# Kernel tuning notes

Measured on AMD Instinct MI355X. Metric: run time of the kernel, lower is better.

The kernel has to match this reference:

```python
import jax, jax.numpy as jnp
import numpy as np

N = 100000
EMB = 64
HID = 64
E = 1600000

def _sage_conv(x, src, dst, w_l, b_l, w_r):
    # PyG SAGEConv (aggr='mean'): out_i = lin_l(mean_{j->i} x_j) + lin_r(x_i)
    msgs = x[src]                                        # [E, d] gather
    agg = jax.ops.segment_sum(msgs, dst, num_segments=N) # [N, d] scatter-add
    deg = jax.ops.segment_sum(jnp.ones((src.shape[0],), x.dtype), dst, num_segments=N)
    agg = agg / jnp.maximum(deg, 1.0)[:, None]           # mean; 0-degree nodes stay 0
    return agg @ w_l.T + b_l + x @ w_r.T                 # lin_l has bias, lin_r does not

def setup_inputs() -> dict:
    key = jax.random.key(0)
    ks = jax.random.split(key, 8)
    emb_std = 1.0 / (EMB ** 0.5)
    # Linear init (Kaiming-uniform-like bounds approximated with uniform +-1/sqrt(fan_in))
    def lin(k, out_d, in_d):
        return jax.random.uniform(k, (out_d, in_d), jnp.float32, -1.0/np.sqrt(in_d), 1.0/np.sqrt(in_d))
    return {
        "embedding": jax.random.normal(ks[0], (N, EMB), jnp.float32) * emb_std,
        "w_l0": lin(ks[1], HID, EMB),
        "b_l0": jax.random.uniform(ks[2], (HID,), jnp.float32, -1.0/np.sqrt(EMB), 1.0/np.sqrt(EMB)),
        "w_r0": lin(ks[3], HID, EMB),
        "w_l1": lin(ks[4], HID, HID),
        "b_l1": jax.random.uniform(ks[5], (HID,), jnp.float32, -1.0/np.sqrt(HID), 1.0/np.sqrt(HID)),
        "w_r1": lin(ks[6], HID, HID),
        "edge_index": jax.random.randint(ks[7], (2, E), 0, N, dtype=jnp.int64),
    }

def reference(embedding, w_l0, b_l0, w_r0, w_l1, b_l1, w_r1, edge_index):
    src, dst = edge_index[0], edge_index[1]
    x = embedding
    x = _sage_conv(x, src, dst, w_l0, b_l0, w_r0)
    x = jax.nn.relu(x)
    x = _sage_conv(x, src, dst, w_l1, b_l1, w_r1)
    # F.normalize(p=2, dim=1): x / clamp_min(||x||_2, 1e-12)
    norm = jnp.sqrt(jnp.sum(x * x, axis=1, keepdims=True))
    return x / jnp.maximum(norm, 1e-12)
```

## Files before the change

kernel.cpp:

```cpp
#include <hip/hip_runtime.h>
#include <math.h>

#define D 64
#define BSHIFT 9
#define BN 512
#define MAXB 256
#define NBLK 256
#define NBLK_LOG 8
#define SCHUNK 4096

typedef short bf16x8v __attribute__((ext_vector_type(8)));
typedef float f32x4v __attribute__((ext_vector_type(4)));

__device__ __forceinline__ unsigned short f2bf(float f) {
    unsigned u = __float_as_uint(f);
    return (unsigned short)((u + 0x7FFFu + ((u >> 16) & 1u)) >> 16);
}
__device__ __forceinline__ float bf2f(unsigned short b) {
    return __uint_as_float(((unsigned)b) << 16);
}

__global__ void detect_idx64(const int* __restrict__ ei, int* __restrict__ flag) {
    int v = ei[2 * threadIdx.x + 1];
    unsigned long long b = __ballot(v != 0);
    if (threadIdx.x == 0) flag[0] = (b == 0ULL) ? 1 : 0;
}

__global__ __launch_bounds__(256) void conv_w4(
        const float* __restrict__ w0, const float* __restrict__ w1,
        const float* __restrict__ w2, const float* __restrict__ w3,
        unsigned short* __restrict__ hi, unsigned short* __restrict__ lo) {
    int i = blockIdx.x * 256 + threadIdx.x;
    const float* ws_[4] = {w0, w1, w2, w3};
    float f = ws_[i >> 12][i & 4095];
    unsigned short h = f2bf(f);
    hi[i] = h;
    lo[i] = f2bf(f - bf2f(h));
}

__global__ __launch_bounds__(256) void conv_xbf(
        const float* __restrict__ x, uint4* __restrict__ xb4, int total8) {
    int i = blockIdx.x * 256 + threadIdx.x;
    int stride = gridDim.x * 256;
    for (; i < total8; i += stride) {
        float4 u0 = *(const float4*)(x + (size_t)i * 8);
        float4 u1 = *(const float4*)(x + (size_t)i * 8 + 4);
        uint4 p;
        p.x = (unsigned)f2bf(u0.x) | ((unsigned)f2bf(u0.y) << 16);
        p.y = (unsigned)f2bf(u0.z) | ((unsigned)f2bf(u0.w) << 16);
        p.z = (unsigned)f2bf(u1.x) | ((unsigned)f2bf(u1.y) << 16);
        p.w = (unsigned)f2bf(u1.z) | ((unsigned)f2bf(u1.w) << 16);
        xb4[i] = p;
    }
}


__global__ __launch_bounds__(256) void hist2d(
        const void* __restrict__ eidx, const int* __restrict__ flagp,
        int* __restrict__ H, int nE, int nb, int epb) {
    __shared__ int h[MAXB];
    const bool idx64 = (*flagp != 0);
    const int* __restrict__ ei32 = (const int*)eidx;
    const long long* __restrict__ ei64 = (const long long*)eidx;
    for (int i = threadIdx.x; i < nb; i += 256) h[i] = 0;
    __syncthreads();
    const int e0 = blockIdx.x * epb;
    const int e1 = min(e0 + epb, nE);
    for (int e = e0 + threadIdx.x; e < e1; e += 256) {
        int d = idx64 ? (int)ei64[e + nE] : ei32[e + nE];
        atomicAdd(&h[d >> BSHIFT], 1);
    }
    __syncthreads();
    for (int i = threadIdx.x; i < nb; i += 256)
        H[(i << NBLK_LOG) + blockIdx.x] = h[i];
}

__global__ __launch_bounds__(256) void scan_h_partial(
        const int* __restrict__ H, int* __restrict__ part, int total) {
    __shared__ int red[4];
    int base = blockIdx.x * SCHUNK + threadIdx.x * 16;
    int s = 0;
    #pragma unroll
    for (int k = 0; k < 16; ++k) { int i = base + k; if (i < total) s += H[i]; }
    #pragma unroll
    for (int off = 32; off >= 1; off >>= 1) s += __shfl_xor(s, off, 64);
    int lane = threadIdx.x & 63, wid = threadIdx.x >> 6;
    if (lane == 0) red[wid] = s;
    __syncthreads();
    if (threadIdx.x == 0) part[blockIdx.x] = red[0] + red[1] + red[2] + red[3];
}

__global__ void scan_h_mid(int* __restrict__ part, int* __restrict__ bbaseN,
                           int nParts, int nE) {
    int tid = threadIdx.x;
    int v = (tid < nParts) ? part[tid] : 0;
    int x = v;
    #pragma unroll
    for (int off = 1; off < 64; off <<= 1) { int y = __shfl_up(x, off, 64); if (tid >= off) x += y; }
    if (tid < nParts) part[tid] = x - v;
    if (tid == 0) bbaseN[0] = nE;
}

__global__ __launch_bounds__(256) void scan_h_final(
        int* __restrict__ H, const int* __restrict__ part,
        int* __restrict__ bbase, int total) {
    __shared__ int wtot[4];
    int tid = threadIdx.x, lane = tid & 63, wid = tid >> 6;
    int base = blockIdx.x * SCHUNK + tid * 16;
    int v[16]; int t = 0;
    #pragma unroll
    for (int k = 0; k < 16; ++k) { int i = base + k; v[k] = (i < total) ? H[i] : 0; t += v[k]; }
    int x = t;
    #pragma unroll
    for (int off = 1; off < 64; off <<= 1) { int y = __shfl_up(x, off, 64); if (lane >= off) x += y; }
    if (lane == 63) wtot[wid] = x;
    __syncthreads();
    int woff = 0;
    for (int w = 0; w < wid; ++w) woff += wtot[w];
    int run = part[blockIdx.x] + woff + (x - t);
    #pragma unroll
    for (int k = 0; k < 16; ++k) {
        int i = base + k;
        if (i < total) {
            H[i] = run;
            if ((i & (NBLK - 1)) == 0) bbase[i >> NBLK_LOG] = run;
            run += v[k];
        }
    }
}

__global__ __launch_bounds__(256) void fill2(
        const void* __restrict__ eidx, const int* __restrict__ flagp,
        const int* __restrict__ H, unsigned* __restrict__ pairs,
        int nE, int nb, int epb) {
    __shared__ int cur[MAXB];
    const bool idx64 = (*flagp != 0);
    const int* __restrict__ ei32 = (const int*)eidx;
    const long long* __restrict__ ei64 = (const long long*)eidx;
    for (int i = threadIdx.x; i < nb; i += 256)
        cur[i] = H[(i << NBLK_LOG) + blockIdx.x];
    __syncthreads();
    const int e0 = blockIdx.x * epb;
    const int e1 = min(e0 + epb, nE);
    for (int e = e0 + threadIdx.x; e < e1; e += 256) {
        int s, d;
        if (idx64) { s = (int)ei64[e]; d = (int)ei64[e + nE]; }
        else       { s = ei32[e];      d = ei32[e + nE]; }
        int pos = atomicAdd(&cur[d >> BSHIFT], 1);
        pairs[pos] = (unsigned)s | ((unsigned)(d & (BN - 1)) << 20);
    }
}

__global__ __launch_bounds__(512) void bucket_to_csr(
        const unsigned* __restrict__ pairs,
        const int* __restrict__ bbase,
        int* __restrict__ rowStart, int* __restrict__ srcs,
        int N, int nb, int nE) {
    __shared__ int lcnt[BN];
    __shared__ int lcur[BN];
    __shared__ int wtot[8];
    const int b = blockIdx.x;
    const int base = bbase[b];
    const int cnt  = bbase[b + 1] - base;
    const int tid = threadIdx.x, lane = tid & 63, wid = tid >> 6;
    lcnt[tid] = 0;
    __syncthreads();
    for (int i = tid; i < cnt; i += 512)
        atomicAdd(&lcnt[(int)(pairs[base + i] >> 20)], 1);
    __syncthreads();
    int v = lcnt[tid];
    int x = v;
    #pragma unroll
    for (int off = 1; off < 64; off <<= 1) { int y = __shfl_up(x, off, 64); if (lane >= off) x += y; }
    if (lane == 63) wtot[wid] = x;
    __syncthreads();
    if (tid == 0) {
        int r = 0;
        for (int w = 0; w < 8; ++w) { int t = wtot[w]; wtot[w] = r; r += t; }
    }
    __syncthreads();
    int excl = wtot[wid] + (x - v);
    lcur[tid] = excl;
    int node = b * BN + tid;
    if (node < N) rowStart[node] = base + excl;
    if (b == nb - 1 && tid == 0) rowStart[N] = nE;
    __syncthreads();
    for (int i = tid; i < cnt; i += 512) {
        unsigned p = pairs[base + i];
        int pos = atomicAdd(&lcur[(int)(p >> 20)], 1);
        srcs[base + pos] = (int)(p & 0xFFFFFu);
    }
}

#define UNPK8(v, arr)                                                     \
    do {                                                                  \
        arr[0] += __uint_as_float((v).x << 16);                           \
        arr[1] += __uint_as_float((v).x & 0xFFFF0000u);                   \
        arr[2] += __uint_as_float((v).y << 16);                           \
        arr[3] += __uint_as_float((v).y & 0xFFFF0000u);                   \
        arr[4] += __uint_as_float((v).z << 16);                           \
        arr[5] += __uint_as_float((v).z & 0xFFFF0000u);                   \
        arr[6] += __uint_as_float((v).w << 16);                           \
        arr[7] += __uint_as_float((v).w & 0xFFFF0000u);                   \
    } while (0)

__global__ __launch_bounds__(256) void gather_mean_bf16(
        const unsigned short* __restrict__ xb,
        const int* __restrict__ rowStart,
        const int* __restrict__ srcs,
        unsigned short* __restrict__ aggb,
        int nNodes) {
    const int tid = threadIdx.x;
    const int gl = tid & 7;
    const int grp = tid >> 3;
    const int node = blockIdx.x * 32 + grp;
    if (node >= nNodes) return;
    const int r0 = rowStart[node], r1 = rowStart[node + 1];
    float a[8] = {0.f,0.f,0.f,0.f,0.f,0.f,0.f,0.f};
    const unsigned short* xp = xb + gl * 8;
    int j = r0;
    for (; j + 4 <= r1; j += 4) {
        int s0 = srcs[j], s1 = srcs[j + 1], s2 = srcs[j + 2], s3 = srcs[j + 3];
        uint4 v0 = *(const uint4*)(xp + (size_t)s0 * D);
        uint4 v1 = *(const uint4*)(xp + (size_t)s1 * D);
        uint4 v2 = *(const uint4*)(xp + (size_t)s2 * D);
        uint4 v3 = *(const uint4*)(xp + (size_t)s3 * D);
        UNPK8(v0, a); UNPK8(v1, a); UNPK8(v2, a); UNPK8(v3, a);
    }
    if (j + 2 <= r1) {
        int s0 = srcs[j], s1 = srcs[j + 1];
        uint4 v0 = *(const uint4*)(xp + (size_t)s0 * D);
        uint4 v1 = *(const uint4*)(xp + (size_t)s1 * D);
        UNPK8(v0, a); UNPK8(v1, a);
        j += 2;
    }
    if (j < r1) {
        uint4 v = *(const uint4*)(xp + (size_t)srcs[j] * D);
        UNPK8(v, a);
    }
    const float inv = 1.0f / fmaxf((float)(r1 - r0), 1.0f);
    uint4 p;
    p.x = (unsigned)f2bf(a[0]*inv) | ((unsigned)f2bf(a[1]*inv) << 16);
    p.y = (unsigned)f2bf(a[2]*inv) | ((unsigned)f2bf(a[3]*inv) << 16);
    p.z = (unsigned)f2bf(a[4]*inv) | ((unsigned)f2bf(a[5]*inv) << 16);
    p.w = (unsigned)f2bf(a[6]*inv) | ((unsigned)f2bf(a[7]*inv) << 16);
    *(uint4*)(aggb + (size_t)node * D + gl * 8) = p;
}

template<int LAYER>
__global__ __launch_bounds__(256) void gemm_mfma(
        const unsigned short* __restrict__ aggb,
        const float* __restrict__ xf,
        const unsigned short* __restrict__ xb,
        const unsigned short* __restrict__ wHi,
        const unsigned short* __restrict__ wLo,
        const float* __restrict__ bl,
        float* __restrict__ outf,
        unsigned short* __restrict__ outb,
        int nNodes) {
    const int l = threadIdx.x & 63;
    const int wv = threadIdx.x >> 6;
    const int col = l & 15, grp = l >> 4;
    const int base0 = blockIdx.x * 128 + wv * 32;
    if (base0 >= nNodes) return;

    bf16x8v gH[2][2], sH[2][2], sL[2][2];
    #pragma unroll
    for (int tt = 0; tt < 2; ++tt) {
        const int anode = min(base0 + tt * 16 + col, nNodes - 1);
        #pragma unroll
        for (int h = 0; h < 2; ++h)
            gH[tt][h] = *(const bf16x8v*)(aggb + (size_t)anode * D + h * 32 + grp * 8);
        if (LAYER == 0) {
            const float* ps = xf + (size_t)anode * D;
            #pragma unroll
            for (int h = 0; h < 2; ++h) {
                const int k0 = h * 32 + grp * 8;
                float4 u0 = *(const float4*)(ps + k0);
                float4 u1 = *(const float4*)(ps + k0 + 4);
                float v[8] = {u0.x, u0.y, u0.z, u0.w, u1.x, u1.y, u1.z, u1.w};
                #pragma unroll
                for (int jj = 0; jj < 8; ++jj) {
                    unsigned short hb = f2bf(v[jj]);
                    sH[tt][h][jj] = (short)hb;
                    sL[tt][h][jj] = (short)f2bf(v[jj] - bf2f(hb));
                }
            }
        } else {
            #pragma unroll
            for (int h = 0; h < 2; ++h)
                sH[tt][h] = *(const bf16x8v*)(xb + (size_t)anode * D + h * 32 + grp * 8);
        }
    }

    f32x4v acc[2][4];
    #pragma unroll
    for (int tt = 0; tt < 2; ++tt)
        #pragma unroll
        for (int t = 0; t < 4; ++t) acc[tt][t] = (f32x4v){0.f, 0.f, 0.f, 0.f};

    #pragma unroll
    for (int t = 0; t < 4; ++t) {
        const unsigned short* whl = wHi + (size_t)(t * 16 + col) * D;
        const unsigned short* wol = wLo + (size_t)(t * 16 + col) * D;
        const unsigned short* whr = whl + 4096;
        const unsigned short* wor = wol + 4096;
        #pragma unroll
        for (int h = 0; h < 2; ++h) {
            const int k0 = h * 32 + grp * 8;
            bf16x8v bh  = *(const bf16x8v*)(whl + k0);
            bf16x8v bo  = *(const bf16x8v*)(wol + k0);
            bf16x8v bh2 = *(const bf16x8v*)(whr + k0);
            bf16x8v bo2 = *(const bf16x8v*)(wor + k0);
            #pragma unroll
            for (int tt = 0; tt < 2; ++tt) {
                acc[tt][t] = __builtin_amdgcn_mfma_f32_16x16x32_bf16(gH[tt][h], bh,  acc[tt][t], 0, 0, 0);
                acc[tt][t] = __builtin_amdgcn_mfma_f32_16x16x32_bf16(gH[tt][h], bo,  acc[tt][t], 0, 0, 0);
                acc[tt][t] = __builtin_amdgcn_mfma_f32_16x16x32_bf16(sH[tt][h], bh2, acc[tt][t], 0, 0, 0);
                if (LAYER == 0)
                    acc[tt][t] = __builtin_amdgcn_mfma_f32_16x16x32_bf16(sL[tt][h], bh2, acc[tt][t], 0, 0, 0);
                acc[tt][t] = __builtin_amdgcn_mfma_f32_16x16x32_bf16(sH[tt][h], bo2, acc[tt][t], 0, 0, 0);
            }
        }
    }

    #pragma unroll
    for (int tt = 0; tt < 2; ++tt) {
        const int base = base0 + tt * 16;
        #pragma unroll
        for (int t = 0; t < 4; ++t) {
            float b = bl[t * 16 + col];
            #pragma unroll
            for (int r = 0; r < 4; ++r) acc[tt][t][r] += b;
        }
        if (LAYER == 0) {
            #pragma unroll
            for (int t = 0; t < 4; ++t)
                #pragma unroll
                for (int r = 0; r < 4; ++r) {
                    int n = base + grp * 4 + r;
                    if (n < nNodes)
                        outb[(size_t)n * D + t * 16 + col] = f2bf(fmaxf(acc[tt][t][r], 0.f));
                }
        } else {
            float ss[4] = {0.f, 0.f, 0.f, 0.f};
            #pragma unroll
            for (int t = 0; t < 4; ++t)
                #pragma unroll
                for (int r = 0; r < 4; ++r) ss[r] += acc[tt][t][r] * acc[tt][t][r];
            #pragma unroll
            for (int r = 0; r < 4; ++r) {
                #pragma unroll
                for (int off = 1; off < 16; off <<= 1) ss[r] += __shfl_xor(ss[r], off, 64);
            }
            float inv[4];
            #pragma unroll
            for (int r = 0; r < 4; ++r) inv[r] = 1.0f / fmaxf(sqrtf(ss[r]), 1e-12f);
            #pragma unroll
            for (int t = 0; t < 4; ++t)
                #pragma unroll
                for (int r = 0; r < 4; ++r) {
                    int n = base + grp * 4 + r;
                    if (n < nNodes)
                        outf[(size_t)n * D + t * 16 + col] = acc[tt][t][r] * inv[r];
                }
        }
    }
}


__global__ __launch_bounds__(256) void sage_scatter(
        const float* __restrict__ x,
        const void* __restrict__ eidx,
        const int* __restrict__ flagp,
        float* __restrict__ agg,
        float* __restrict__ deg,
        int nE, int doDeg) {
    const bool idx64 = (*flagp != 0);
    const int lane = threadIdx.x & 63;
    int wave = (int)((blockIdx.x * blockDim.x + threadIdx.x) >> 6);
    const int waveStride = (int)((gridDim.x * blockDim.x) >> 6);
    const int* __restrict__ ei32 = (const int*)eidx;
    const long long* __restrict__ ei64 = (const long long*)eidx;
    for (int e = wave; e < nE; e += waveStride) {
        int s, d;
        if (idx64) { s = (int)ei64[e]; d = (int)ei64[e + nE]; }
        else       { s = ei32[e];      d = ei32[e + nE]; }
        atomicAdd(&agg[(size_t)d * D + lane], x[(size_t)s * D + lane]);
        if (doDeg && lane == 0) atomicAdd(&deg[d], 1.0f);
    }
}

__global__ __launch_bounds__(256) void sage_update(
        const float* __restrict__ xin,
        const float* __restrict__ agg,
        const float* __restrict__ deg,
        const float* __restrict__ wl,
        const float* __restrict__ bl,
        const float* __restrict__ wr,
        float* __restrict__ xout,
        int nNodes, int mode) {
    __shared__ float wlT[D * D];
    __shared__ float wrT[D * D];
    __shared__ float rowA[4][D];
    __shared__ float rowX[4][D];
    for (int i = threadIdx.x; i < D * D; i += blockDim.x) {
        int f = i >> 6, k = i & 63;
        wlT[k * D + f] = wl[i];
        wrT[k * D + f] = wr[i];
    }
    __syncthreads();
    const int lane = threadIdx.x & 63;
    const int wid = threadIdx.x >> 6;
    const float blv = bl[lane];
    for (int node = blockIdx.x * 4 + wid; node < nNodes; node += gridDim.x * 4) {
        float dg = fmaxf(deg[node], 1.0f);
        float a  = agg[(size_t)node * D + lane] / dg;
        float xv = xin[(size_t)node * D + lane];
        rowA[wid][lane] = a;
        rowX[wid][lane] = xv;
        float acc = blv;
        #pragma unroll
        for (int k = 0; k < D; ++k) {
            acc = fmaf(rowA[wid][k], wlT[k * D + lane], acc);
            acc = fmaf(rowX[wid][k], wrT[k * D + lane], acc);
        }
        if (mode == 0) {
            xout[(size_t)node * D + lane] = fmaxf(acc, 0.0f);
        } else {
            float ss = acc * acc;
            #pragma unroll
            for (int off = 32; off >= 1; off >>= 1) ss += __shfl_xor(ss, off, 64);
            xout[(size_t)node * D + lane] = acc / fmaxf(sqrtf(ss), 1e-12f);
        }
    }
}

extern "C" void kernel_launch(void* const* d_in, const int* in_sizes, int n_in,
                              void* d_out, int out_size, void* d_ws, size_t ws_size,
                              hipStream_t stream) {
    const float* x   = (const float*)d_in[0];
    const float* wl0 = (const float*)d_in[1];
    const float* bl0 = (const float*)d_in[2];
    const float* wr0 = (const float*)d_in[3];
    const float* wl1 = (const float*)d_in[4];
    const float* bl1 = (const float*)d_in[5];
    const float* wr1 = (const float*)d_in[6];
    const void*  ei  = d_in[7];
    float* out = (float*)d_out;

    const int N = in_sizes[0] / D;
    const int E = in_sizes[7] / 2;
    const int NB = (N + BN - 1) / BN;
    const int EPB = (E + NBLK - 1) / NBLK;
    const int TOTAL = NB << NBLK_LOG;
    const int NPARTS = (TOTAL + SCHUNK - 1) / SCHUNK;

    char* ws = (char*)d_ws;
    size_t off = 0;
    auto alloc = [&](size_t bytes) { void* p = ws + off; off = (off + bytes + 255) & ~(size_t)255; return p; };

    size_t regionA_bytes = (size_t)E * 4;
    if ((size_t)N * D * 2 > regionA_bytes) regionA_bytes = (size_t)N * D * 2;
    size_t need = 0;
    {
        size_t o = 0;
        auto sim = [&](size_t b) { o = (o + b + 255) & ~(size_t)255; };
        sim(4); sim(16384 * 2); sim(16384 * 2);
        sim(((size_t)MAXB << NBLK_LOG) * 4); sim(64 * 4); sim(((size_t)MAXB + 1) * 4);
        sim(((size_t)N + 1) * 4); sim((size_t)E * 4);
        sim(regionA_bytes); sim((size_t)N * D * 2); sim((size_t)N * D * 2);
        need = o;
    }

    if (ws_size >= need && NB <= MAXB && NPARTS <= 64) {
        int* flag     = (int*)alloc(4);
        unsigned short* whi = (unsigned short*)alloc(16384 * 2);
        unsigned short* wlo = (unsigned short*)alloc(16384 * 2);
        int* H        = (int*)alloc(((size_t)MAXB << NBLK_LOG) * 4);
        int* part     = (int*)alloc(64 * 4);
        int* bbase    = (int*)alloc(((size_t)MAXB + 1) * 4);
        int* rowStart = (int*)alloc(((size_t)N + 1) * 4);
        int* srcs     = (int*)alloc((size_t)E * 4);
        void* regionA = alloc(regionA_bytes);
        unsigned short* x1b  = (unsigned short*)alloc((size_t)N * D * 2);
        unsigned short* aggb = (unsigned short*)alloc((size_t)N * D * 2);
        unsigned* pairs = (unsigned*)regionA;
        unsigned short* xb = (unsigned short*)regionA;

        detect_idx64<<<1, 64, 0, stream>>>((const int*)ei, flag);
        conv_w4<<<64, 256, 0, stream>>>(wl0, wr0, wl1, wr1, whi, wlo);
        hist2d<<<NBLK, 256, 0, stream>>>(ei, flag, H, E, NB, EPB);
        scan_h_partial<<<NPARTS, 256, 0, stream>>>(H, part, TOTAL);
        scan_h_mid<<<1, 64, 0, stream>>>(part, &bbase[NB], NPARTS, E);
        scan_h_final<<<NPARTS, 256, 0, stream>>>(H, part, bbase, TOTAL);
        fill2<<<NBLK, 256, 0, stream>>>(ei, flag, H, pairs, E, NB, EPB);
        bucket_to_csr<<<NB, 512, 0, stream>>>(pairs, bbase, rowStart, srcs, N, NB, E);
        conv_xbf<<<1024, 256, 0, stream>>>(x, (uint4*)xb, N * 8);

        const int gGather = (N + 31) / 32;
        const int gMfma   = (N + 127) / 128;
        gather_mean_bf16<<<gGather, 256, 0, stream>>>(xb, rowStart, srcs, aggb, N);
        gemm_mfma<0><<<gMfma, 256, 0, stream>>>(aggb, x, (const unsigned short*)0,
                                                whi, wlo, bl0, (float*)0, x1b, N);
        gather_mean_bf16<<<gGather, 256, 0, stream>>>(x1b, rowStart, srcs, aggb, N);
        gemm_mfma<1><<<gMfma, 256, 0, stream>>>(aggb, (const float*)0, x1b,
                                                whi + 2 * 4096, wlo + 2 * 4096, bl1,
                                                out, (unsigned short*)0, N);
    } else {
        int*   flag = (int*)alloc(4);
        float* deg  = (float*)alloc((size_t)N * 4);
        float* agg  = (float*)alloc((size_t)N * D * 4);
        float* x1   = out;

        detect_idx64<<<1, 64, 0, stream>>>((const int*)ei, flag);
        hipMemsetAsync(deg, 0, ((size_t)N + (size_t)N * D) * 4, stream);
        sage_scatter<<<4096, 256, 0, stream>>>(x, ei, flag, agg, deg, E, 1);
        sage_update<<<2048, 256, 0, stream>>>(x, agg, deg, wl0, bl0, wr0, x1, N, 0);
        hipMemsetAsync(agg, 0, (size_t)N * D * 4, stream);
        sage_scatter<<<4096, 256, 0, stream>>>(x1, ei, flag, agg, deg, E, 0);
        sage_update<<<2048, 256, 0, stream>>>(x1, agg, deg, wl1, bl1, wr1, out, N, 1);
    }
}
```

Before: 178.7 us.

## Fuse prep kernels, shrink CSR buckets, unroll gather, use bf16 self-features

Merges index-width detection, weight hi/lo splitting and x-to-bf16 conversion into one prep launch, which saves launches and lets the conversion run before CSR build. It separates the pairs and xb buffers so they no longer alias. Bucket size drops from 512 to 256 nodes per bucket, so bucket_to_csr uses 256-thread blocks over more buckets. The gather loop is unrolled to 8 neighbours per iteration to keep more loads in flight. Layer 0's GEMM now reads the bf16 copy of x instead of splitting fp32 into hi/lo, which removes one MFMA per step and the in-kernel conversion but loses accuracy on the root term.

```diff
diff --git a/kernel.cpp b/kernel.cpp
--- a/kernel.cpp
+++ b/kernel.cpp
@@ -2,9 +2,9 @@
 #include <math.h>
 
 #define D 64
-#define BSHIFT 9
-#define BN 512
-#define MAXB 256
+#define BSHIFT 8
+#define BN 256
+#define MAXB 512
 #define NBLK 256
 #define NBLK_LOG 8
 #define SCHUNK 4096
@@ -20,28 +20,33 @@
     return __uint_as_float(((unsigned)b) << 16);
 }
 
-__global__ void detect_idx64(const int* __restrict__ ei, int* __restrict__ flag) {
-    int v = ei[2 * threadIdx.x + 1];
-    unsigned long long b = __ballot(v != 0);
-    if (threadIdx.x == 0) flag[0] = (b == 0ULL) ? 1 : 0;
-}
-
-__global__ __launch_bounds__(256) void conv_w4(
+__global__ __launch_bounds__(256) void prep(
+        const int* __restrict__ ei, int* __restrict__ flag,
         const float* __restrict__ w0, const float* __restrict__ w1,
         const float* __restrict__ w2, const float* __restrict__ w3,
-        unsigned short* __restrict__ hi, unsigned short* __restrict__ lo) {
-    int i = blockIdx.x * 256 + threadIdx.x;
-    const float* ws_[4] = {w0, w1, w2, w3};
-    float f = ws_[i >> 12][i & 4095];
-    unsigned short h = f2bf(f);
-    hi[i] = h;
-    lo[i] = f2bf(f - bf2f(h));
-}
-
-__global__ __launch_bounds__(256) void conv_xbf(
-        const float* __restrict__ x, uint4* __restrict__ xb4, int total8) {
-    int i = blockIdx.x * 256 + threadIdx.x;
-    int stride = gridDim.x * 256;
+        unsigned short* __restrict__ hi, unsigned short* __restrict__ lo,
+        const float* __restrict__ x, uint4* __restrict__ xb4, int total8,
+        int nXbfBlocks) {
+    const int b = blockIdx.x;
+    if (b == 0) {
+        if (threadIdx.x < 64) {
+            int v = ei[2 * threadIdx.x + 1];
+            unsigned long long m = __ballot(v != 0);
+            if (threadIdx.x == 0) flag[0] = (m == 0ULL) ? 1 : 0;
+        }
+        return;
+    }
+    if (b < 65) {
+        int i = (b - 1) * 256 + threadIdx.x;
+        const float* ws_[4] = {w0, w1, w2, w3};
+        float f = ws_[i >> 12][i & 4095];
+        unsigned short h = f2bf(f);
+        hi[i] = h;
+        lo[i] = f2bf(f - bf2f(h));
+        return;
+    }
+    int i = (b - 65) * 256 + threadIdx.x;
+    int stride = nXbfBlocks * 256;
     for (; i < total8; i += stride) {
         float4 u0 = *(const float4*)(x + (size_t)i * 8);
         float4 u1 = *(const float4*)(x + (size_t)i * 8 + 4);
@@ -151,21 +156,21 @@
     }
 }
 
-__global__ __launch_bounds__(512) void bucket_to_csr(
+__global__ __launch_bounds__(256) void bucket_to_csr(
         const unsigned* __restrict__ pairs,
         const int* __restrict__ bbase,
         int* __restrict__ rowStart, int* __restrict__ srcs,
         int N, int nb, int nE) {
     __shared__ int lcnt[BN];
     __shared__ int lcur[BN];
-    __shared__ int wtot[8];
+    __shared__ int wtot[4];
     const int b = blockIdx.x;
     const int base = bbase[b];
     const int cnt  = bbase[b + 1] - base;
     const int tid = threadIdx.x, lane = tid & 63, wid = tid >> 6;
     lcnt[tid] = 0;
     __syncthreads();
-    for (int i = tid; i < cnt; i += 512)
+    for (int i = tid; i < cnt; i += 256)
         atomicAdd(&lcnt[(int)(pairs[base + i] >> 20)], 1);
     __syncthreads();
     int v = lcnt[tid];
@@ -176,7 +181,7 @@
     __syncthreads();
     if (tid == 0) {
         int r = 0;
-        for (int w = 0; w < 8; ++w) { int t = wtot[w]; wtot[w] = r; r += t; }
+        for (int w = 0; w < 4; ++w) { int t = wtot[w]; wtot[w] = r; r += t; }
     }
     __syncthreads();
     int excl = wtot[wid] + (x - v);
@@ -185,7 +190,7 @@
     if (node < N) rowStart[node] = base + excl;
     if (b == nb - 1 && tid == 0) rowStart[N] = nE;
     __syncthreads();
-    for (int i = tid; i < cnt; i += 512) {
+    for (int i = tid; i < cnt; i += 256) {
         unsigned p = pairs[base + i];
         int pos = atomicAdd(&lcur[(int)(p >> 20)], 1);
         srcs[base + pos] = (int)(p & 0xFFFFFu);
@@ -219,18 +224,29 @@
     float a[8] = {0.f,0.f,0.f,0.f,0.f,0.f,0.f,0.f};
     const unsigned short* xp = xb + gl * 8;
     int j = r0;
-    for (; j + 4 <= r1; j += 4) {
-        int s0 = srcs[j], s1 = srcs[j + 1], s2 = srcs[j + 2], s3 = srcs[j + 3];
-        uint4 v0 = *(const uint4*)(xp + (size_t)s0 * D);
-        uint4 v1 = *(const uint4*)(xp + (size_t)s1 * D);
-        uint4 v2 = *(const uint4*)(xp + (size_t)s2 * D);
-        uint4 v3 = *(const uint4*)(xp + (size_t)s3 * D);
+    for (; j + 8 <= r1; j += 8) {
+        uint4 v0 = *(const uint4*)(xp + (size_t)srcs[j    ] * D);
+        uint4 v1 = *(const uint4*)(xp + (size_t)srcs[j + 1] * D);
+        uint4 v2 = *(const uint4*)(xp + (size_t)srcs[j + 2] * D);
+        uint4 v3 = *(const uint4*)(xp + (size_t)srcs[j + 3] * D);
+        uint4 v4 = *(const uint4*)(xp + (size_t)srcs[j + 4] * D);
+        uint4 v5 = *(const uint4*)(xp + (size_t)srcs[j + 5] * D);
+        uint4 v6 = *(const uint4*)(xp + (size_t)srcs[j + 6] * D);
+        uint4 v7 = *(const uint4*)(xp + (size_t)srcs[j + 7] * D);
         UNPK8(v0, a); UNPK8(v1, a); UNPK8(v2, a); UNPK8(v3, a);
+        UNPK8(v4, a); UNPK8(v5, a); UNPK8(v6, a); UNPK8(v7, a);
+    }
+    if (j + 4 <= r1) {
+        uint4 v0 = *(const uint4*)(xp + (size_t)srcs[j    ] * D);
+        uint4 v1 = *(const uint4*)(xp + (size_t)srcs[j + 1] * D);
+        uint4 v2 = *(const uint4*)(xp + (size_t)srcs[j + 2] * D);
+        uint4 v3 = *(const uint4*)(xp + (size_t)srcs[j + 3] * D);
+        UNPK8(v0, a); UNPK8(v1, a); UNPK8(v2, a); UNPK8(v3, a);
+        j += 4;
     }
     if (j + 2 <= r1) {
-        int s0 = srcs[j], s1 = srcs[j + 1];
-        uint4 v0 = *(const uint4*)(xp + (size_t)s0 * D);
-        uint4 v1 = *(const uint4*)(xp + (size_t)s1 * D);
+        uint4 v0 = *(const uint4*)(xp + (size_t)srcs[j    ] * D);
+        uint4 v1 = *(const uint4*)(xp + (size_t)srcs[j + 1] * D);
         UNPK8(v0, a); UNPK8(v1, a);
         j += 2;
     }
@@ -250,8 +266,7 @@
 template<int LAYER>
 __global__ __launch_bounds__(256) void gemm_mfma(
         const unsigned short* __restrict__ aggb,
-        const float* __restrict__ xf,
-        const unsigned short* __restrict__ xb,
+        const unsigned short* __restrict__ xin,
         const unsigned short* __restrict__ wHi,
         const unsigned short* __restrict__ wLo,
         const float* __restrict__ bl,
@@ -264,32 +279,14 @@
     const int base0 = blockIdx.x * 128 + wv * 32;
     if (base0 >= nNodes) return;
 
-    bf16x8v gH[2][2], sH[2][2], sL[2][2];
+    bf16x8v gH[2][2], sH[2][2];
     #pragma unroll
     for (int tt = 0; tt < 2; ++tt) {
         const int anode = min(base0 + tt * 16 + col, nNodes - 1);
         #pragma unroll
-        for (int h = 0; h < 2; ++h)
+        for (int h = 0; h < 2; ++h) {
             gH[tt][h] = *(const bf16x8v*)(aggb + (size_t)anode * D + h * 32 + grp * 8);
-        if (LAYER == 0) {
-            const float* ps = xf + (size_t)anode * D;
-            #pragma unroll
-            for (int h = 0; h < 2; ++h) {
-                const int k0 = h * 32 + grp * 8;
-                float4 u0 = *(const float4*)(ps + k0);
-                float4 u1 = *(const float4*)(ps + k0 + 4);
-                float v[8] = {u0.x, u0.y, u0.z, u0.w, u1.x, u1.y, u1.z, u1.w};
-                #pragma unroll
-                for (int jj = 0; jj < 8; ++jj) {
-                    unsigned short hb = f2bf(v[jj]);
-                    sH[tt][h][jj] = (short)hb;
-                    sL[tt][h][jj] = (short)f2bf(v[jj] - bf2f(hb));
-                }
-            }
-        } else {
-            #pragma unroll
-            for (int h = 0; h < 2; ++h)
-                sH[tt][h] = *(const bf16x8v*)(xb + (size_t)anode * D + h * 32 + grp * 8);
+            sH[tt][h] = *(const bf16x8v*)(xin  + (size_t)anode * D + h * 32 + grp * 8);
         }
     }
 
@@ -317,8 +314,6 @@
                 acc[tt][t] = __builtin_amdgcn_mfma_f32_16x16x32_bf16(gH[tt][h], bh,  acc[tt][t], 0, 0, 0);
                 acc[tt][t] = __builtin_amdgcn_mfma_f32_16x16x32_bf16(gH[tt][h], bo,  acc[tt][t], 0, 0, 0);
                 acc[tt][t] = __builtin_amdgcn_mfma_f32_16x16x32_bf16(sH[tt][h], bh2, acc[tt][t], 0, 0, 0);
-                if (LAYER == 0)
-                    acc[tt][t] = __builtin_amdgcn_mfma_f32_16x16x32_bf16(sL[tt][h], bh2, acc[tt][t], 0, 0, 0);
                 acc[tt][t] = __builtin_amdgcn_mfma_f32_16x16x32_bf16(sH[tt][h], bo2, acc[tt][t], 0, 0, 0);
             }
         }
@@ -368,6 +363,12 @@
     }
 }
 
+
+__global__ void detect_idx64(const int* __restrict__ ei, int* __restrict__ flag) {
+    int v = ei[2 * threadIdx.x + 1];
+    unsigned long long b = __ballot(v != 0);
+    if (threadIdx.x == 0) flag[0] = (b == 0ULL) ? 1 : 0;
+}
 
 __global__ __launch_bounds__(256) void sage_scatter(
         const float* __restrict__ x,
@@ -460,16 +461,14 @@
     size_t off = 0;
     auto alloc = [&](size_t bytes) { void* p = ws + off; off = (off + bytes + 255) & ~(size_t)255; return p; };
 
-    size_t regionA_bytes = (size_t)E * 4;
-    if ((size_t)N * D * 2 > regionA_bytes) regionA_bytes = (size_t)N * D * 2;
     size_t need = 0;
     {
         size_t o = 0;
         auto sim = [&](size_t b) { o = (o + b + 255) & ~(size_t)255; };
         sim(4); sim(16384 * 2); sim(16384 * 2);
         sim(((size_t)MAXB << NBLK_LOG) * 4); sim(64 * 4); sim(((size_t)MAXB + 1) * 4);
-        sim(((size_t)N + 1) * 4); sim((size_t)E * 4);
-        sim(regionA_bytes); sim((size_t)N * D * 2); sim((size_t)N * D * 2);
+        sim(((size_t)N + 1) * 4); sim((size_t)E * 4); sim((size_t)E * 4);
+        sim((size_t)N * D * 2); sim((size_t)N * D * 2); sim((size_t)N * D * 2);
         need = o;
     }
 
@@ -482,31 +481,30 @@
         int* bbase    = (int*)alloc(((size_t)MAXB + 1) * 4);
         int* rowStart = (int*)alloc(((size_t)N + 1) * 4);
         int* srcs     = (int*)alloc((size_t)E * 4);
-        void* regionA = alloc(regionA_bytes);
+        unsigned* pairs = (unsigned*)alloc((size_t)E * 4);
+        unsigned short* xb   = (unsigned short*)alloc((size_t)N * D * 2);
         unsigned short* x1b  = (unsigned short*)alloc((size_t)N * D * 2);
         unsigned short* aggb = (unsigned short*)alloc((size_t)N * D * 2);
-        unsigned* pairs = (unsigned*)regionA;
-        unsigned short* xb = (unsigned short*)regionA;
-
-        detect_idx64<<<1, 64, 0, stream>>>((const int*)ei, flag);
-        conv_w4<<<64, 256, 0, stream>>>(wl0, wr0, wl1, wr1, whi, wlo);
+
+        const int nXbf = 1024;
+        prep<<<65 + nXbf, 256, 0, stream>>>((const int*)ei, flag,
+                                            wl0, wr0, wl1, wr1, whi, wlo,
+                                            x, (uint4*)xb, N * 8, nXbf);
         hist2d<<<NBLK, 256, 0, stream>>>(ei, flag, H, E, NB, EPB);
         scan_h_partial<<<NPARTS, 256, 0, stream>>>(H, part, TOTAL);
         scan_h_mid<<<1, 64, 0, stream>>>(part, &bbase[NB], NPARTS, E);
         scan_h_final<<<NPARTS, 256, 0, stream>>>(H, part, bbase, TOTAL);
         fill2<<<NBLK, 256, 0, stream>>>(ei, flag, H, pairs, E, NB, EPB);
-        bucket_to_csr<<<NB, 512, 0, stream>>>(pairs, bbase, rowStart, srcs, N, NB, E);
-        conv_xbf<<<1024, 256, 0, stream>>>(x, (uint4*)xb, N * 8);
+        bucket_to_csr<<<NB, 256, 0, stream>>>(pairs, bbase, rowStart, srcs, N, NB, E);
 
         const int gGather = (N + 31) / 32;
         const int gMfma   = (N + 127) / 128;
         gather_mean_bf16<<<gGather, 256, 0, stream>>>(xb, rowStart, srcs, aggb, N);
-        gemm_mfma<0><<<gMfma, 256, 0, stream>>>(aggb, x, (const unsigned short*)0,
-                                                whi, wlo, bl0, (float*)0, x1b, N);
+        gemm_mfma<0><<<gMfma, 256, 0, stream>>>(aggb, xb, whi, wlo, bl0,
+                                                (float*)0, x1b, N);
         gather_mean_bf16<<<gGather, 256, 0, stream>>>(x1b, rowStart, srcs, aggb, N);
-        gemm_mfma<1><<<gMfma, 256, 0, stream>>>(aggb, (const float*)0, x1b,
-                                                whi + 2 * 4096, wlo + 2 * 4096, bl1,
-                                                out, (unsigned short*)0, N);
+        gemm_mfma<1><<<gMfma, 256, 0, stream>>>(aggb, x1b, whi + 2 * 4096, wlo + 2 * 4096,
+                                                bl1, out, (unsigned short*)0, N);
     } else {
         int*   flag = (int*)alloc(4);
         float* deg  = (float*)alloc((size_t)N * 4);
```

New measurement: 169.8 us. 1.05x faster.
